# Optimization experiments

Measured on AMD Instinct MI355X. Metric: run time of the kernel, lower is better.

Reference implementation:

```python
import jax, jax.numpy as jnp
import numpy as np

B = 64          # batch_size
N_PER = 1000    # num_nodes per graph
NTOT = B * N_PER
H = 64          # hidden_gnn_dim


def _gcn_aggregate(x, senders, receivers, add_self_edges):
    """jraph.GraphConvolution aggregation with symmetric normalization.
    x: [NTOT, F] node features AFTER update_node_fn."""
    if add_self_edges:
        self_idx = jnp.arange(NTOT, dtype=senders.dtype)
        s = jnp.concatenate([senders, self_idx])
        r = jnp.concatenate([receivers, self_idx])
    else:
        s, r = senders, receivers
    ones = jnp.ones_like(s, dtype=x.dtype)
    deg_s = jax.ops.segment_sum(ones, s, num_segments=NTOT)
    deg_r = jax.ops.segment_sum(ones, r, num_segments=NTOT)
    x = x * jax.lax.rsqrt(jnp.maximum(deg_s, 1.0))[:, None]
    x = jax.ops.segment_sum(x[s], r, num_segments=NTOT)
    x = x * jax.lax.rsqrt(jnp.maximum(deg_r, 1.0))[:, None]
    return x


def setup_inputs() -> dict:
    key = jax.random.key(0)
    ks = jax.random.split(key, 12)
    n_edges = 1_000_000
    in_dim, fc, lat, out_dim = 64, 512, 64, 32
    flat = N_PER * H  # 64000

    def w(k, shape, fan_in):
        return jax.random.normal(k, shape, dtype=jnp.float32) / np.sqrt(fan_in)

    return {
        "nodes": jax.random.normal(ks[0], (NTOT, in_dim), dtype=jnp.float32),
        "senders": jax.random.randint(ks[1], (n_edges,), 0, NTOT),
        "receivers": jax.random.randint(ks[2], (n_edges,), 0, NTOT),
        "eps": jax.random.normal(ks[3], (B, lat), dtype=jnp.float32),
        "W_gcn1": w(ks[4], (in_dim, H), in_dim),
        "b_gcn1": jnp.zeros((H,), jnp.float32),
        "W_fc": w(ks[5], (flat, fc), flat),
        "b_fc": jnp.zeros((fc,), jnp.float32),
        "W_mean": w(ks[6], (fc, lat), fc),
        "b_mean": jnp.zeros((lat,), jnp.float32),
        "W_logstd": w(ks[7], (fc, lat), fc),
        "b_logstd": jnp.zeros((lat,), jnp.float32),
        "W_dec_fc": w(ks[8], (lat, flat), lat),
        "b_dec_fc": jnp.zeros((flat,), jnp.float32),
        "W_dec_out": w(ks[9], (H, out_dim), H),
        "b_dec_out": jnp.zeros((out_dim,), jnp.float32),
    }


def reference(nodes, senders, receivers, eps, W_gcn1, b_gcn1, W_fc, b_fc,
              W_mean, b_mean, W_logstd, b_logstd, W_dec_fc, b_dec_fc,
              W_dec_out, b_dec_out):
    # --- Encoder: GCN(update=Linear+relu, add_self_edges=True) ---
    h = jax.nn.relu(nodes @ W_gcn1 + b_gcn1)                 # [NTOT, H]
    h = _gcn_aggregate(h, senders, receivers, add_self_edges=True)
    x = h.reshape(B, N_PER * H)                              # flatten per graph
    x = jax.nn.relu(x @ W_fc + b_fc)                         # [B, fc]
    mean = x @ W_mean + b_mean                               # [B, lat]
    log_std = x @ W_logstd + b_logstd                        # [B, lat]
    # --- Reparameterization ---
    z = mean + jnp.exp(log_std) * eps                        # [B, lat]
    # --- Decoder ---
    d = jax.nn.relu(z @ W_dec_fc + b_dec_fc)                 # [B, N_PER*H]
    d = d.reshape(NTOT, H)
    d = d @ W_dec_out + b_dec_out                            # update_node_fn
    out_nodes = _gcn_aggregate(d, senders, receivers, add_self_edges=False)
    return mean, log_std, out_nodes
```

## Files before the change

kernel.cpp:

```cpp
#include <hip/hip_runtime.h>
#include <math.h>

#define NTOT 64000
#define HD   64
#define NB   64
#define FC   512
#define LAT  64
#define OUTD 32
#define GKC  256
#define NKB  250
#define NBH  64
#define NBUK 250
#define BSH  8

typedef __bf16 bf16x8 __attribute__((ext_vector_type(8)));
typedef float  f32x4  __attribute__((ext_vector_type(4)));

__device__ inline float bflo(unsigned u) { union {unsigned q; float f;} x; x.q = u << 16; return x.f; }
__device__ inline float bfhi(unsigned u) { union {unsigned q; float f;} x; x.q = u & 0xFFFF0000u; return x.f; }
__device__ inline unsigned pkbf(float lo, float hi) {
  __bf16 a = (__bf16)lo, b = (__bf16)hi;
  unsigned short ua, ub;
  __builtin_memcpy(&ua, &a, 2); __builtin_memcpy(&ub, &b, 2);
  return (unsigned)ua | ((unsigned)ub << 16);
}

__global__ __launch_bounds__(256) void k_hist(const int* __restrict__ s,
    const int* __restrict__ r, unsigned* __restrict__ partials, int nE) {
  __shared__ unsigned hist[16000];
  int arr = blockIdx.y;
  const int* idx = arr ? r : s;
  unsigned* base = partials + ((size_t)arr * NBH + blockIdx.x) * 16000;
  for (int u = threadIdx.x; u < 16000; u += 256) hist[u] = 0;
  __syncthreads();
  int chunk = (nE + NBH - 1) / NBH;
  int e0 = blockIdx.x * chunk;
  int e1 = min(e0 + chunk, nE);
  for (int e = e0 + threadIdx.x; e < e1; e += 256) {
    int i = idx[e];
    atomicAdd(&hist[i >> 2], 1u << ((i & 3) * 8));
  }
  __syncthreads();
  for (int u = threadIdx.x; u < 16000; u += 256) base[u] = hist[u];
}

__global__ __launch_bounds__(128) void k_sum(const unsigned* __restrict__ partials,
    int* __restrict__ dout, int* __restrict__ din) {
  int t = blockIdx.x * 128 + threadIdx.x;
  unsigned a = 0, b = 0;
  for (int bk = 0; bk < NBH; bk++) {
    a += partials[(size_t)bk * 16000 + t];
    b += partials[((size_t)NBH + bk) * 16000 + t];
  }
  int4 va = make_int4(a & 255, (a >> 8) & 255, (a >> 16) & 255, a >> 24);
  int4 vb = make_int4(b & 255, (b >> 8) & 255, (b >> 16) & 255, b >> 24);
  *reinterpret_cast<int4*>(dout + t * 4) = va;
  *reinterpret_cast<int4*>(din + t * 4) = vb;
}

__global__ void k_scan1(const int* __restrict__ din, int* __restrict__ rs,
                        int* __restrict__ bsums) {
  __shared__ int sm[256];
  int i = blockIdx.x * 256 + threadIdx.x;
  int v = din[i];
  sm[threadIdx.x] = v;
  __syncthreads();
  for (int d = 1; d < 256; d <<= 1) {
    int t = (threadIdx.x >= d) ? sm[threadIdx.x - d] : 0;
    __syncthreads();
    sm[threadIdx.x] += t;
    __syncthreads();
  }
  rs[i] = sm[threadIdx.x] - v;
  if (threadIdx.x == 255) bsums[blockIdx.x] = sm[255];
}

__global__ void k_scan2(int* __restrict__ rs, int* __restrict__ gcur,
                        const int* __restrict__ bsums, int nE) {
  __shared__ int sm[256];
  int bid = blockIdx.x, t = threadIdx.x;
  sm[t] = (t < bid) ? bsums[t] : 0;
  __syncthreads();
  for (int d = 128; d > 0; d >>= 1) {
    if (t < d) sm[t] += sm[t + d];
    __syncthreads();
  }
  int i = bid * 256 + t;
  int v = rs[i] + sm[0];
  rs[i] = v;
  if ((i & 255) == 0) gcur[i >> 8] = v;
  if (bid == 0 && t == 0) rs[NTOT] = nE;
}

__global__ __launch_bounds__(256) void k_bucket(const int* __restrict__ s,
    const int* __restrict__ r, int* __restrict__ gcur,
    unsigned* __restrict__ ebuf, int nE) {
  __shared__ int cnt[NBUK];
  __shared__ int base[NBUK];
  int tid = threadIdx.x;
  int chunk = (nE + gridDim.x - 1) / gridDim.x;
  int e0 = blockIdx.x * chunk;
  int e1 = min(e0 + chunk, nE);
  for (int u = tid; u < NBUK; u += 256) cnt[u] = 0;
  __syncthreads();
  for (int e = e0 + tid; e < e1; e += 256)
    atomicAdd(&cnt[r[e] >> BSH], 1);
  __syncthreads();
  for (int u = tid; u < NBUK; u += 256) {
    base[u] = atomicAdd(&gcur[u], cnt[u]);
    cnt[u] = 0;
  }
  __syncthreads();
  for (int e = e0 + tid; e < e1; e += 256) {
    int rr = r[e];
    int b = rr >> BSH;
    int off = atomicAdd(&cnt[b], 1);
    ebuf[base[b] + off] = ((unsigned)(rr & 255) << 16) | (unsigned)s[e];
  }
}

__global__ __launch_bounds__(256) void k_fill2(const unsigned* __restrict__ ebuf,
    const int* __restrict__ rs, int* __restrict__ csr) {
  __shared__ int cur[256];
  int b = blockIdx.x;
  int tid = threadIdx.x;
  int nbase = b << BSH;
  cur[tid] = rs[nbase + tid];
  __syncthreads();
  int e0 = rs[nbase];
  int e1 = rs[nbase + 256];
  for (int e = e0 + tid; e < e1; e += 256) {
    unsigned p = ebuf[e];
    int pos = atomicAdd(&cur[p >> 16], 1);
    csr[pos] = (int)(p & 0xFFFFu);
  }
}

__global__ __launch_bounds__(256) void k_node1(const float* __restrict__ nodes,
    const float* __restrict__ W1, const float* __restrict__ b1,
    const int* __restrict__ dout, __bf16* __restrict__ h1) {
  __shared__ float wsm[HD * HD];
  int tid = threadIdx.x;
  for (int u = tid; u < HD * HD; u += 256) wsm[u] = W1[u];
  __syncthreads();
  int node = blockIdx.x * 4 + (tid >> 6);
  int f = tid & 63;
  const float* xr = nodes + (size_t)node * HD;
  float acc = b1[f];
#pragma unroll 16
  for (int k = 0; k < HD; k++) acc = fmaf(xr[k], wsm[k * HD + f], acc);
  acc = fmaxf(acc, 0.f);
  h1[(size_t)node * HD + f] = (__bf16)(acc * rsqrtf((float)(dout[node] + 1)));
}

__global__ __launch_bounds__(256) void k_agg1(const unsigned* __restrict__ h1u,
    const int* __restrict__ rs, const int* __restrict__ csr,
    const int* __restrict__ din, unsigned* __restrict__ xbo) {
  int tid = threadIdx.x;
  int node = blockIdx.x * 8 + (tid >> 5);
  int f2 = tid & 31;
  int beg = rs[node], end = rs[node + 1];
  unsigned su = h1u[node * 32 + f2];
  float a0 = bflo(su), b0 = bfhi(su);
  float a1 = 0, b1 = 0, a2 = 0, b2 = 0, a3 = 0, b3 = 0;
  int e = beg;
  for (; e + 4 <= end; e += 4) {
    unsigned u0 = h1u[csr[e] * 32 + f2];
    unsigned u1 = h1u[csr[e + 1] * 32 + f2];
    unsigned u2 = h1u[csr[e + 2] * 32 + f2];
    unsigned u3 = h1u[csr[e + 3] * 32 + f2];
    a0 += bflo(u0); b0 += bfhi(u0);
    a1 += bflo(u1); b1 += bfhi(u1);
    a2 += bflo(u2); b2 += bfhi(u2);
    a3 += bflo(u3); b3 += bfhi(u3);
  }
  for (; e < end; e++) {
    unsigned u = h1u[csr[e] * 32 + f2];
    a1 += bflo(u); b1 += bfhi(u);
  }
  float sc = rsqrtf((float)(din[node] + 1));
  xbo[node * 32 + f2] = pkbf(((a0 + a1) + (a2 + a3)) * sc, ((b0 + b1) + (b2 + b3)) * sc);
}

__global__ __launch_bounds__(512) void k_gemm(const __bf16* __restrict__ xb,
    const float* __restrict__ Wfc, float* __restrict__ part) {
  __shared__ __align__(16) __bf16 As[64 * 264];
  int kb = blockIdx.x;
  int k0 = kb * GKC;
  int tid = threadIdx.x;
  for (int u = tid; u < 64 * 32; u += 512) {
    int row = u >> 5, c = u & 31;
    const uint4* src = reinterpret_cast<const uint4*>(xb + (size_t)row * 64000 + k0);
    reinterpret_cast<uint4*>(&As[row * 264])[c] = src[c];
  }
  __syncthreads();
  int w = tid >> 6, lane = tid & 63;
  int cw = lane & 15, kg = lane >> 4;
  const float* Bp = Wfc + ((size_t)k0 + kg * 8) * FC + w * 64 + cw;
  f32x4 acc[4][4];
#pragma unroll
  for (int mt = 0; mt < 4; mt++)
#pragma unroll
    for (int nt = 0; nt < 4; nt++) acc[mt][nt] = (f32x4){0.f, 0.f, 0.f, 0.f};

  for (int ks = 0; ks < 8; ks++) {
    bf16x8 bfrag[4];
#pragma unroll
    for (int nt = 0; nt < 4; nt++) {
      const float* bp = Bp + (size_t)ks * 32 * FC + nt * 16;
      bf16x8 bb;
#pragma unroll
      for (int b = 0; b < 8; b++) bb[b] = (__bf16)bp[(size_t)b * FC];
      bfrag[nt] = bb;
    }
    bf16x8 afrag[4];
#pragma unroll
    for (int mt = 0; mt < 4; mt++)
      afrag[mt] = *reinterpret_cast<const bf16x8*>(
          &As[(mt * 16 + cw) * 264 + ks * 32 + kg * 8]);
#pragma unroll
    for (int mt = 0; mt < 4; mt++)
#pragma unroll
      for (int nt = 0; nt < 4; nt++)
        acc[mt][nt] = __builtin_amdgcn_mfma_f32_16x16x32_bf16(
            afrag[mt], bfrag[nt], acc[mt][nt], 0, 0, 0);
  }
#pragma unroll
  for (int mt = 0; mt < 4; mt++)
#pragma unroll
    for (int nt = 0; nt < 4; nt++) {
      int col = w * 64 + nt * 16 + cw;
#pragma unroll
      for (int j = 0; j < 4; j++) {
        int row = mt * 16 + kg * 4 + j;
        part[((size_t)kb * 64 + row) * FC + col] = acc[mt][nt][j];
      }
    }
}

__global__ __launch_bounds__(256) void k_reduce(const float* __restrict__ part,
    const float* __restrict__ bfc, float* __restrict__ xf) {
  __shared__ float sm[256];
  int t = threadIdx.x;
  int i = blockIdx.x * 128 + (t & 127);
  int half = t >> 7;
  float sv = 0.f;
  int kb0 = half * (NKB / 2);
  int kb1 = kb0 + (NKB / 2);
  for (int kb = kb0; kb < kb1; kb++) sv += part[(size_t)kb * (NB * FC) + i];
  sm[t] = sv;
  __syncthreads();
  if (half == 0)
    xf[i] = fmaxf(sm[t] + sm[t + 128] + bfc[i & (FC - 1)], 0.f);
}

__global__ __launch_bounds__(256) void k_head(const float* __restrict__ xf,
    const float* __restrict__ Wm, const float* __restrict__ bm,
    const float* __restrict__ Wl, const float* __restrict__ bl,
    const float* __restrict__ eps, float* __restrict__ out_mean,
    float* __restrict__ out_logstd, float* __restrict__ z) {
  __shared__ float xr[FC];
  __shared__ float ps[4][LAT];
  __shared__ float zm[LAT];
  int b = blockIdx.x, t = threadIdx.x;
  for (int u = t; u < FC; u += 256) xr[u] = xf[b * FC + u];
  __syncthreads();
  int g = t >> 6;
  int l = t & 63;
  int h = g & 1;
  const float* W = (g < 2) ? Wm : Wl;
  float acc = 0.f;
  int kb = h * (FC / 2);
#pragma unroll 8
  for (int k = kb; k < kb + FC / 2; k++) acc = fmaf(xr[k], W[k * LAT + l], acc);
  ps[g][l] = acc;
  __syncthreads();
  float ls = 0.f;
  if (g == 0) {
    float m = ps[0][l] + ps[1][l] + bm[l];
    out_mean[b * 64 + l] = m;
    zm[l] = m;
  }
  if (g == 2) {
    ls = ps[2][l] + ps[3][l] + bl[l];
    out_logstd[b * 64 + l] = ls;
  }
  __syncthreads();
  if (g == 2) z[b * 64 + l] = zm[l] + expf(ls) * eps[b * 64 + l];
}

__global__ __launch_bounds__(256) void k_dec_fc(const float* __restrict__ z,
    const float* __restrict__ Wdf, const float* __restrict__ bdf,
    __bf16* __restrict__ dbuf) {
  __shared__ float zs[NB * LAT];
  int tid = threadIdx.x;
  for (int u = tid; u < NB * LAT; u += 256) zs[u] = z[u];
  __syncthreads();
  int j = blockIdx.x * 32 + (tid & 31);
  int b0 = (tid >> 5) * 8;
  float bias = bdf[j];
  float acc[8];
#pragma unroll
  for (int i = 0; i < 8; i++) acc[i] = bias;
  for (int k = 0; k < LAT; k++) {
    float w = Wdf[(size_t)k * 64000 + j];
#pragma unroll
    for (int i = 0; i < 8; i++) acc[i] = fmaf(zs[(b0 + i) * LAT + k], w, acc[i]);
  }
#pragma unroll
  for (int i = 0; i < 8; i++)
    dbuf[(size_t)(b0 + i) * 64000 + j] = (__bf16)fmaxf(acc[i], 0.f);
}

__global__ __launch_bounds__(256) void k_dec_out(const __bf16* __restrict__ dbuf,
    const float* __restrict__ Wdo, const float* __restrict__ bdo,
    const int* __restrict__ dout, __bf16* __restrict__ dds) {
  __shared__ float wsm[HD * OUTD];
  __shared__ float dr[8][HD];
  int tid = threadIdx.x;
  for (int u = tid; u < HD * OUTD; u += 256) wsm[u] = Wdo[u];
  int node0 = blockIdx.x * 8;
  {
    int nl = tid >> 5, k = tid & 31;
    dr[nl][k]      = (float)dbuf[(size_t)(node0 + nl) * HD + k];
    dr[nl][k + 32] = (float)dbuf[(size_t)(node0 + nl) * HD + k + 32];
  }
  __syncthreads();
  int nl = tid >> 5, f = tid & 31;
  int node = node0 + nl;
  float acc = bdo[f];
#pragma unroll 8
  for (int k = 0; k < HD; k++) acc = fmaf(dr[nl][k], wsm[k * OUTD + f], acc);
  dds[(size_t)node * OUTD + f] = (__bf16)(acc * rsqrtf(fmaxf((float)dout[node], 1.f)));
}

__global__ __launch_bounds__(256) void k_agg2(const unsigned* __restrict__ ddsu,
    const int* __restrict__ rs, const int* __restrict__ csr,
    const int* __restrict__ din, float* __restrict__ outn) {
  int tid = threadIdx.x;
  int node = blockIdx.x * 16 + (tid >> 4);
  int f2 = tid & 15;
  int beg = rs[node], end = rs[node + 1];
  float a0 = 0, b0 = 0, a1 = 0, b1 = 0, a2 = 0, b2 = 0, a3 = 0, b3 = 0;
  int e = beg;
  for (; e + 4 <= end; e += 4) {
    unsigned u0 = ddsu[csr[e] * 16 + f2];
    unsigned u1 = ddsu[csr[e + 1] * 16 + f2];
    unsigned u2 = ddsu[csr[e + 2] * 16 + f2];
    unsigned u3 = ddsu[csr[e + 3] * 16 + f2];
    a0 += bflo(u0); b0 += bfhi(u0);
    a1 += bflo(u1); b1 += bfhi(u1);
    a2 += bflo(u2); b2 += bfhi(u2);
    a3 += bflo(u3); b3 += bfhi(u3);
  }
  for (; e < end; e++) {
    unsigned u = ddsu[csr[e] * 16 + f2];
    a1 += bflo(u); b1 += bfhi(u);
  }
  float sc = rsqrtf(fmaxf((float)din[node], 1.f));
  float2 o = make_float2(((a0 + a1) + (a2 + a3)) * sc, ((b0 + b1) + (b2 + b3)) * sc);
  *reinterpret_cast<float2*>(outn + (size_t)node * 32 + f2 * 2) = o;
}

extern "C" void kernel_launch(void* const* d_in, const int* in_sizes, int n_in,
                              void* d_out, int out_size, void* d_ws, size_t ws_size,
                              hipStream_t stream) {
  const float* nodes   = (const float*)d_in[0];
  const int*   senders = (const int*)d_in[1];
  const int*   recvs   = (const int*)d_in[2];
  const float* eps     = (const float*)d_in[3];
  const float* W1      = (const float*)d_in[4];
  const float* b1      = (const float*)d_in[5];
  const float* Wfc     = (const float*)d_in[6];
  const float* bfc     = (const float*)d_in[7];
  const float* Wm      = (const float*)d_in[8];
  const float* bm      = (const float*)d_in[9];
  const float* Wl      = (const float*)d_in[10];
  const float* bl      = (const float*)d_in[11];
  const float* Wdf     = (const float*)d_in[12];
  const float* bdf     = (const float*)d_in[13];
  const float* Wdo     = (const float*)d_in[14];
  const float* bdo     = (const float*)d_in[15];
  int nE = in_sizes[1];

  char* w = (char*)d_ws;
  auto alloc = [&](size_t bytes) {
    char* p = w;
    w += (bytes + 255) & ~(size_t)255;
    return p;
  };
  int* deg_out   = (int*)alloc((size_t)NTOT * 4);
  int* deg_in    = (int*)alloc((size_t)NTOT * 4);
  int* row_start = (int*)alloc((size_t)(NTOT + 1) * 4);
  int* gcur      = (int*)alloc((size_t)NBUK * 4);
  int* bsums     = (int*)alloc(256 * 4);
  int* csr       = (int*)alloc((size_t)nE * 4);
  unsigned* ebuf = (unsigned*)alloc((size_t)nE * 4);
  __bf16* h1  = (__bf16*)alloc((size_t)NTOT * HD * 2);
  __bf16* xb  = (__bf16*)alloc((size_t)NTOT * HD * 2);
  float* part = (float*)alloc((size_t)NKB * NB * FC * 4);
  float* xf   = (float*)alloc((size_t)NB * FC * 4);
  float* z    = (float*)alloc((size_t)NB * LAT * 4);
  __bf16* dbuf = h1;
  __bf16* dds  = xb;
  unsigned* partials = (unsigned*)part;

  float* out_mean   = (float*)d_out;
  float* out_logstd = (float*)d_out + 4096;
  float* out_nodes  = (float*)d_out + 8192;

  k_hist<<<dim3(NBH, 2), 256, 0, stream>>>(senders, recvs, partials, nE);
  k_sum<<<125, 128, 0, stream>>>(partials, deg_out, deg_in);
  k_scan1<<<NTOT / 256, 256, 0, stream>>>(deg_in, row_start, bsums);
  k_scan2<<<NTOT / 256, 256, 0, stream>>>(row_start, gcur, bsums, nE);
  k_bucket<<<256, 256, 0, stream>>>(senders, recvs, gcur, ebuf, nE);
  k_fill2<<<NBUK, 256, 0, stream>>>(ebuf, row_start, csr);
  k_node1<<<NTOT / 4, 256, 0, stream>>>(nodes, W1, b1, deg_out, h1);
  k_agg1<<<NTOT / 8, 256, 0, stream>>>((const unsigned*)h1, row_start, csr, deg_in, (unsigned*)xb);
  k_gemm<<<NKB, 512, 0, stream>>>(xb, Wfc, part);
  k_reduce<<<NB * FC / 128, 256, 0, stream>>>(part, bfc, xf);
  k_head<<<NB, 256, 0, stream>>>(xf, Wm, bm, Wl, bl, eps, out_mean, out_logstd, z);
  k_dec_fc<<<64000 / 32, 256, 0, stream>>>(z, Wdf, bdf, dbuf);
  k_dec_out<<<NTOT / 8, 256, 0, stream>>>(dbuf, Wdo, bdo, deg_out, dds);
  k_agg2<<<NTOT / 16, 256, 0, stream>>>((const unsigned*)dds, row_start, csr, deg_in, out_nodes);
}
```

Measured before the change: 249.8 us.

## Fuse degree sum into scan, fuse decoder GEMMs, split edges across lanes in aggregation

Merges the degree-summing kernel into the first scan kernel and doubles the number of histogram blocks. Fuses the decoder FC and output projection into one kernel per node position so the intermediate decoder activations never go to global memory. The aggregation kernels now split each node's edge list across 2 or 4 lane groups and combine the partial sums with cross-lane shuffles, and node1 processes 16 nodes per block. The goal is fewer launches, less memory traffic and more parallelism in the gathers. In exchange, reductions use more partial buffers and the fused decoder kernel uses about 65KB of shared memory per block, which may limit occupancy.

```diff
diff --git a/kernel.cpp b/kernel.cpp
--- a/kernel.cpp
+++ b/kernel.cpp
@@ -9,7 +9,7 @@
 #define OUTD 32
 #define GKC  256
 #define NKB  250
-#define NBH  64
+#define NBH  128
 #define NBUK 250
 #define BSH  8
 
@@ -44,35 +44,35 @@
   for (int u = threadIdx.x; u < 16000; u += 256) base[u] = hist[u];
 }
 
-__global__ __launch_bounds__(128) void k_sum(const unsigned* __restrict__ partials,
+__global__ __launch_bounds__(256) void k_scan1(const unsigned* __restrict__ partials,
+    int* __restrict__ rs, int* __restrict__ bsums,
     int* __restrict__ dout, int* __restrict__ din) {
-  int t = blockIdx.x * 128 + threadIdx.x;
-  unsigned a = 0, b = 0;
-  for (int bk = 0; bk < NBH; bk++) {
-    a += partials[(size_t)bk * 16000 + t];
-    b += partials[((size_t)NBH + bk) * 16000 + t];
-  }
-  int4 va = make_int4(a & 255, (a >> 8) & 255, (a >> 16) & 255, a >> 24);
-  int4 vb = make_int4(b & 255, (b >> 8) & 255, (b >> 16) & 255, b >> 24);
-  *reinterpret_cast<int4*>(dout + t * 4) = va;
-  *reinterpret_cast<int4*>(din + t * 4) = vb;
-}
-
-__global__ void k_scan1(const int* __restrict__ din, int* __restrict__ rs,
-                        int* __restrict__ bsums) {
   __shared__ int sm[256];
-  int i = blockIdx.x * 256 + threadIdx.x;
-  int v = din[i];
-  sm[threadIdx.x] = v;
+  __shared__ unsigned bw[64];
+  int t = threadIdx.x;
+  int w0 = blockIdx.x * 64;
+  if (t < 64) {
+    unsigned a = 0, b = 0;
+    for (int bk = 0; bk < NBH; bk++) a += partials[(size_t)bk * 16000 + w0 + t];
+    for (int bk = 0; bk < NBH; bk++) b += partials[((size_t)NBH + bk) * 16000 + w0 + t];
+    bw[t] = b;
+    *reinterpret_cast<int4*>(dout + (size_t)(w0 + t) * 4) =
+        make_int4(a & 255, (a >> 8) & 255, (a >> 16) & 255, a >> 24);
+    *reinterpret_cast<int4*>(din + (size_t)(w0 + t) * 4) =
+        make_int4(b & 255, (b >> 8) & 255, (b >> 16) & 255, b >> 24);
+  }
+  __syncthreads();
+  int v = (int)((bw[t >> 2] >> ((t & 3) * 8)) & 255u);
+  sm[t] = v;
   __syncthreads();
   for (int d = 1; d < 256; d <<= 1) {
-    int t = (threadIdx.x >= d) ? sm[threadIdx.x - d] : 0;
+    int x = (t >= d) ? sm[t - d] : 0;
     __syncthreads();
-    sm[threadIdx.x] += t;
+    sm[t] += x;
     __syncthreads();
   }
-  rs[i] = sm[threadIdx.x] - v;
-  if (threadIdx.x == 255) bsums[blockIdx.x] = sm[255];
+  rs[blockIdx.x * 256 + t] = sm[t] - v;
+  if (t == 255) bsums[blockIdx.x] = sm[255];
 }
 
 __global__ void k_scan2(int* __restrict__ rs, int* __restrict__ gcur,
@@ -143,43 +143,42 @@
   int tid = threadIdx.x;
   for (int u = tid; u < HD * HD; u += 256) wsm[u] = W1[u];
   __syncthreads();
-  int node = blockIdx.x * 4 + (tid >> 6);
-  int f = tid & 63;
-  const float* xr = nodes + (size_t)node * HD;
-  float acc = b1[f];
+  int f = tid & 63, g = tid >> 6;
+#pragma unroll
+  for (int it = 0; it < 4; it++) {
+    int node = blockIdx.x * 16 + it * 4 + g;
+    const float* xr = nodes + (size_t)node * HD;
+    float acc = b1[f];
 #pragma unroll 16
-  for (int k = 0; k < HD; k++) acc = fmaf(xr[k], wsm[k * HD + f], acc);
-  acc = fmaxf(acc, 0.f);
-  h1[(size_t)node * HD + f] = (__bf16)(acc * rsqrtf((float)(dout[node] + 1)));
+    for (int k = 0; k < HD; k++) acc = fmaf(xr[k], wsm[k * HD + f], acc);
+    acc = fmaxf(acc, 0.f);
+    h1[(size_t)node * HD + f] = (__bf16)(acc * rsqrtf((float)(dout[node] + 1)));
+  }
 }
 
 __global__ __launch_bounds__(256) void k_agg1(const unsigned* __restrict__ h1u,
     const int* __restrict__ rs, const int* __restrict__ csr,
     const int* __restrict__ din, unsigned* __restrict__ xbo) {
   int tid = threadIdx.x;
-  int node = blockIdx.x * 8 + (tid >> 5);
-  int f2 = tid & 31;
+  int node = blockIdx.x * 4 + (tid >> 6);
+  int lane = tid & 63;
+  int f2 = lane & 31, eo = lane >> 5;
   int beg = rs[node], end = rs[node + 1];
-  unsigned su = h1u[node * 32 + f2];
-  float a0 = bflo(su), b0 = bfhi(su);
-  float a1 = 0, b1 = 0, a2 = 0, b2 = 0, a3 = 0, b3 = 0;
-  int e = beg;
-  for (; e + 4 <= end; e += 4) {
-    unsigned u0 = h1u[csr[e] * 32 + f2];
-    unsigned u1 = h1u[csr[e + 1] * 32 + f2];
-    unsigned u2 = h1u[csr[e + 2] * 32 + f2];
-    unsigned u3 = h1u[csr[e + 3] * 32 + f2];
-    a0 += bflo(u0); b0 += bfhi(u0);
-    a1 += bflo(u1); b1 += bfhi(u1);
-    a2 += bflo(u2); b2 += bfhi(u2);
-    a3 += bflo(u3); b3 += bfhi(u3);
-  }
-  for (; e < end; e++) {
-    unsigned u = h1u[csr[e] * 32 + f2];
-    a1 += bflo(u); b1 += bfhi(u);
-  }
-  float sc = rsqrtf((float)(din[node] + 1));
-  xbo[node * 32 + f2] = pkbf(((a0 + a1) + (a2 + a3)) * sc, ((b0 + b1) + (b2 + b3)) * sc);
+  float a = 0.f, b = 0.f;
+  if (eo == 0) {
+    unsigned su = h1u[(size_t)node * 32 + f2];
+    a = bflo(su); b = bfhi(su);
+  }
+  for (int e = beg + eo; e < end; e += 2) {
+    unsigned u = h1u[(size_t)csr[e] * 32 + f2];
+    a += bflo(u); b += bfhi(u);
+  }
+  a += __shfl_xor(a, 32, 64);
+  b += __shfl_xor(b, 32, 64);
+  if (eo == 0) {
+    float sc = rsqrtf((float)(din[node] + 1));
+    xbo[(size_t)node * 32 + f2] = pkbf(a * sc, b * sc);
+  }
 }
 
 __global__ __launch_bounds__(512) void k_gemm(const __bf16* __restrict__ xb,
@@ -289,77 +288,69 @@
   if (g == 2) z[b * 64 + l] = zm[l] + expf(ls) * eps[b * 64 + l];
 }
 
-__global__ __launch_bounds__(256) void k_dec_fc(const float* __restrict__ z,
+__global__ __launch_bounds__(256) void k_dec(const float* __restrict__ z,
     const float* __restrict__ Wdf, const float* __restrict__ bdf,
-    __bf16* __restrict__ dbuf) {
-  __shared__ float zs[NB * LAT];
-  int tid = threadIdx.x;
-  for (int u = tid; u < NB * LAT; u += 256) zs[u] = z[u];
-  __syncthreads();
-  int j = blockIdx.x * 32 + (tid & 31);
-  int b0 = (tid >> 5) * 8;
-  float bias = bdf[j];
-  float acc[8];
-#pragma unroll
-  for (int i = 0; i < 8; i++) acc[i] = bias;
-  for (int k = 0; k < LAT; k++) {
-    float w = Wdf[(size_t)k * 64000 + j];
-#pragma unroll
-    for (int i = 0; i < 8; i++) acc[i] = fmaf(zs[(b0 + i) * LAT + k], w, acc[i]);
-  }
-#pragma unroll
-  for (int i = 0; i < 8; i++)
-    dbuf[(size_t)(b0 + i) * 64000 + j] = (__bf16)fmaxf(acc[i], 0.f);
-}
-
-__global__ __launch_bounds__(256) void k_dec_out(const __bf16* __restrict__ dbuf,
     const float* __restrict__ Wdo, const float* __restrict__ bdo,
-    const int* __restrict__ dout, __bf16* __restrict__ dds) {
-  __shared__ float wsm[HD * OUTD];
-  __shared__ float dr[8][HD];
-  int tid = threadIdx.x;
-  for (int u = tid; u < HD * OUTD; u += 256) wsm[u] = Wdo[u];
-  int node0 = blockIdx.x * 8;
+    const int* __restrict__ deg, __bf16* __restrict__ dds) {
+  __shared__ float zs[64 * 64];
+  __shared__ float ws[64 * 65];
+  __shared__ float ps[64 * 65];
+  __shared__ float wo[64 * 32];
+  int np = blockIdx.x, tid = threadIdx.x;
+  for (int u = tid; u < 4096; u += 256) zs[u] = z[u];
+  for (int u = tid; u < 4096; u += 256)
+    ws[(u >> 6) * 65 + (u & 63)] = Wdf[(size_t)(u >> 6) * 64000 + np * 64 + (u & 63)];
+  for (int u = tid; u < 2048; u += 256) wo[u] = Wdo[u];
+  __syncthreads();
   {
-    int nl = tid >> 5, k = tid & 31;
-    dr[nl][k]      = (float)dbuf[(size_t)(node0 + nl) * HD + k];
-    dr[nl][k + 32] = (float)dbuf[(size_t)(node0 + nl) * HD + k + 32];
-  }
-  __syncthreads();
-  int nl = tid >> 5, f = tid & 31;
-  int node = node0 + nl;
-  float acc = bdo[f];
+    int h = tid & 63, bg = tid >> 6;
+    float bias = bdf[np * 64 + h];
+#pragma unroll
+    for (int bb = 0; bb < 16; bb++) {
+      int b = bg * 16 + bb;
+      float acc = bias;
 #pragma unroll 8
-  for (int k = 0; k < HD; k++) acc = fmaf(dr[nl][k], wsm[k * OUTD + f], acc);
-  dds[(size_t)node * OUTD + f] = (__bf16)(acc * rsqrtf(fmaxf((float)dout[node], 1.f)));
+      for (int k = 0; k < 64; k++) acc = fmaf(zs[b * 64 + k], ws[k * 65 + h], acc);
+      ps[b * 65 + h] = fmaxf(acc, 0.f);
+    }
+  }
+  __syncthreads();
+  {
+    int o = tid & 31, bg = tid >> 5;
+    float bias = bdo[o];
+#pragma unroll
+    for (int bb = 0; bb < 8; bb++) {
+      int b = bg * 8 + bb;
+      float acc = bias;
+#pragma unroll 8
+      for (int h = 0; h < 64; h++) acc = fmaf(ps[b * 65 + h], wo[h * 32 + o], acc);
+      int node = b * 1000 + np;
+      dds[(size_t)node * OUTD + o] =
+          (__bf16)(acc * rsqrtf(fmaxf((float)deg[node], 1.f)));
+    }
+  }
 }
 
 __global__ __launch_bounds__(256) void k_agg2(const unsigned* __restrict__ ddsu,
     const int* __restrict__ rs, const int* __restrict__ csr,
     const int* __restrict__ din, float* __restrict__ outn) {
   int tid = threadIdx.x;
-  int node = blockIdx.x * 16 + (tid >> 4);
-  int f2 = tid & 15;
+  int node = blockIdx.x * 4 + (tid >> 6);
+  int lane = tid & 63;
+  int f2 = lane & 15, eo = lane >> 4;
   int beg = rs[node], end = rs[node + 1];
-  float a0 = 0, b0 = 0, a1 = 0, b1 = 0, a2 = 0, b2 = 0, a3 = 0, b3 = 0;
-  int e = beg;
-  for (; e + 4 <= end; e += 4) {
-    unsigned u0 = ddsu[csr[e] * 16 + f2];
-    unsigned u1 = ddsu[csr[e + 1] * 16 + f2];
-    unsigned u2 = ddsu[csr[e + 2] * 16 + f2];
-    unsigned u3 = ddsu[csr[e + 3] * 16 + f2];
-    a0 += bflo(u0); b0 += bfhi(u0);
-    a1 += bflo(u1); b1 += bfhi(u1);
-    a2 += bflo(u2); b2 += bfhi(u2);
-    a3 += bflo(u3); b3 += bfhi(u3);
-  }
-  for (; e < end; e++) {
-    unsigned u = ddsu[csr[e] * 16 + f2];
-    a1 += bflo(u); b1 += bfhi(u);
-  }
-  float sc = rsqrtf(fmaxf((float)din[node], 1.f));
-  float2 o = make_float2(((a0 + a1) + (a2 + a3)) * sc, ((b0 + b1) + (b2 + b3)) * sc);
-  *reinterpret_cast<float2*>(outn + (size_t)node * 32 + f2 * 2) = o;
+  float a = 0.f, b = 0.f;
+  for (int e = beg + eo; e < end; e += 4) {
+    unsigned u = ddsu[(size_t)csr[e] * 16 + f2];
+    a += bflo(u); b += bfhi(u);
+  }
+  a += __shfl_xor(a, 16, 64); b += __shfl_xor(b, 16, 64);
+  a += __shfl_xor(a, 32, 64); b += __shfl_xor(b, 32, 64);
+  if (eo == 0) {
+    float sc = rsqrtf(fmaxf((float)din[node], 1.f));
+    *reinterpret_cast<float2*>(outn + (size_t)node * 32 + f2 * 2) =
+        make_float2(a * sc, b * sc);
+  }
 }
 
 extern "C" void kernel_launch(void* const* d_in, const int* in_sizes, int n_in,
@@ -401,7 +392,6 @@
   float* part = (float*)alloc((size_t)NKB * NB * FC * 4);
   float* xf   = (float*)alloc((size_t)NB * FC * 4);
   float* z    = (float*)alloc((size_t)NB * LAT * 4);
-  __bf16* dbuf = h1;
   __bf16* dds  = xb;
   unsigned* partials = (unsigned*)part;
 
@@ -410,17 +400,15 @@
   float* out_nodes  = (float*)d_out + 8192;
 
   k_hist<<<dim3(NBH, 2), 256, 0, stream>>>(senders, recvs, partials, nE);
-  k_sum<<<125, 128, 0, stream>>>(partials, deg_out, deg_in);
-  k_scan1<<<NTOT / 256, 256, 0, stream>>>(deg_in, row_start, bsums);
+  k_scan1<<<NTOT / 256, 256, 0, stream>>>(partials, row_start, bsums, deg_out, deg_in);
   k_scan2<<<NTOT / 256, 256, 0, stream>>>(row_start, gcur, bsums, nE);
   k_bucket<<<256, 256, 0, stream>>>(senders, recvs, gcur, ebuf, nE);
   k_fill2<<<NBUK, 256, 0, stream>>>(ebuf, row_start, csr);
-  k_node1<<<NTOT / 4, 256, 0, stream>>>(nodes, W1, b1, deg_out, h1);
-  k_agg1<<<NTOT / 8, 256, 0, stream>>>((const unsigned*)h1, row_start, csr, deg_in, (unsigned*)xb);
+  k_node1<<<NTOT / 16, 256, 0, stream>>>(nodes, W1, b1, deg_out, h1);
+  k_agg1<<<NTOT / 4, 256, 0, stream>>>((const unsigned*)h1, row_start, csr, deg_in, (unsigned*)xb);
   k_gemm<<<NKB, 512, 0, stream>>>(xb, Wfc, part);
   k_reduce<<<NB * FC / 128, 256, 0, stream>>>(part, bfc, xf);
   k_head<<<NB, 256, 0, stream>>>(xf, Wm, bm, Wl, bl, eps, out_mean, out_logstd, z);
-  k_dec_fc<<<64000 / 32, 256, 0, stream>>>(z, Wdf, bdf, dbuf);
-  k_dec_out<<<NTOT / 8, 256, 0, stream>>>(dbuf, Wdo, bdo, deg_out, dds);
-  k_agg2<<<NTOT / 16, 256, 0, stream>>>((const unsigned*)dds, row_start, csr, deg_in, out_nodes);
-}
+  k_dec<<<1000, 256, 0, stream>>>(z, Wdf, bdf, Wdo, bdo, deg_out, dds);
+  k_agg2<<<NTOT / 4, 256, 0, stream>>>((const unsigned*)dds, row_start, csr, deg_in, out_nodes);
+}
```

Result: slower. 295.0 us (+18.1%).
